# Kernel optimization log

Hardware: AMD Instinct MI355X
Metric: run time of the kernel (lower is better)

The kernel has to match this reference:

```python
import jax, jax.numpy as jnp
import numpy as np

FS = 5  # filter_size


def _extract_patches(x, fs):
    """x: (B, C, H, W) -> (B, C, fs*fs, H, W), 'same' padding, row-major
    shift order matching conv2d with an identity (one-hot) kernel."""
    B, C, H, W = x.shape
    pad = fs // 2
    xp = jnp.pad(x, ((0, 0), (0, 0), (pad, pad), (pad, pad)))
    shifts = [xp[:, :, i:i + H, j:j + W] for i in range(fs) for j in range(fs)]
    return jnp.stack(shifts, axis=2)


def setup_inputs() -> dict:
    key = jax.random.key(0)
    k1, k2 = jax.random.split(key)
    B, C, H, W = 8, 32, 128, 128
    x = jax.random.normal(k1, (B, C, H, W), dtype=jnp.float32)
    # PPDFGen modeled as a per-pixel linear map C -> fs^2 (1x1 conv) + bias
    w_gen = jax.random.normal(k2, (FS * FS, C), dtype=jnp.float32) * (1.0 / np.sqrt(C))
    b_gen = jnp.zeros((FS * FS,), dtype=jnp.float32)
    return {"x": x, "w_gen": w_gen, "b_gen": b_gen}


def reference(x, w_gen, b_gen):
    # Per-pixel dynamic filters: (B, fs^2, H, W)
    filters = jnp.einsum('bchw,fc->bfhw', x, w_gen) + b_gen[None, :, None, None]
    # Shifted patches (im2col via identity-kernel conv in the original):
    patches = _extract_patches(x, FS)            # (B, C, fs^2, H, W)
    # Elementwise multiply by filters (broadcast over channels) and reduce
    # over the fs^2 tap axis -- same math as the per-channel loop + concat.
    out = jnp.einsum('bcfhw,bfhw->bchw', patches, filters)
    return out
```

## Files before the change

### kernel.cpp

```cpp
#include <hip/hip_runtime.h>

#define FS   5
#define NTAP 25
#define Bc   8
#define Cc   32
#define Hc   128
#define Wc   128
#define HW   (Hc * Wc)

#define TH      8
#define TW      64
#define HALO_H  (TH + 4)
#define HALO_W  (TW + 4)
#define PLANE   (HALO_H * HALO_W)
#define NPAIR   (PLANE / 2)
#define LDS_BYTES (Cc * PLANE * 4)

__global__ __launch_bounds__(256, 1) void ppdfn_fused_kernel(
    const float* __restrict__ x, const float* __restrict__ wg,
    const float* __restrict__ bg, float* __restrict__ out)
{
    extern __shared__ float xs[];

    const int tid = threadIdx.x;
    const int ht  = blockIdx.x;
    const int wt  = blockIdx.y;
    const int b   = blockIdx.z;
    const int h0  = ht * TH;
    const int w0  = wt * TW;

    int  goff[2];
    bool val[2];
    bool st1;
#pragma unroll
    for (int k = 0; k < 2; ++k) {
        const int ip = tid + k * 256;
        const int i  = ip * 2;
        const int r  = i / HALO_W;
        const int cw = i - r * HALO_W;
        const int gh = h0 - 2 + r;
        const int gw = w0 - 2 + cw;
        val[k]  = (ip < NPAIR) && ((unsigned)gh < (unsigned)Hc) &&
                  ((unsigned)gw < (unsigned)Wc);
        goff[k] = gh * Wc + gw;
    }
    st1 = (tid < NPAIR - 256);

    const float* xb = x + (size_t)b * Cc * HW;

    for (int c = 0; c < Cc; ++c) {
        const float* xc = xb + (size_t)c * HW;
        float2 v0 = make_float2(0.f, 0.f), v1 = make_float2(0.f, 0.f);
        if (val[0]) v0 = *reinterpret_cast<const float2*>(xc + goff[0]);
        if (val[1]) v1 = *reinterpret_cast<const float2*>(xc + goff[1]);
        float* p = xs + c * PLANE;
        *reinterpret_cast<float2*>(p + 2 * tid) = v0;
        if (st1) *reinterpret_cast<float2*>(p + 2 * (tid + 256)) = v1;
    }
    __syncthreads();

    const int ty = tid >> 5;
    const int tx = tid & 31;
    const int w2 = tx * 2;

    float2 f[NTAP];
#pragma unroll
    for (int t = 0; t < NTAP; ++t) {
        const float bv = bg[t];
        f[t].x = bv; f[t].y = bv;
    }
#pragma unroll 2
    for (int c = 0; c < Cc; ++c) {
        const float2 xv = *reinterpret_cast<const float2*>(
            xs + c * PLANE + (ty + 2) * HALO_W + (w2 + 2));
#pragma unroll
        for (int t = 0; t < NTAP; ++t) {
            const float wv = wg[t * Cc + c];
            f[t].x = fmaf(wv, xv.x, f[t].x);
            f[t].y = fmaf(wv, xv.y, f[t].y);
        }
    }

    float* ob = out + (size_t)b * Cc * HW + (h0 + ty) * Wc + (w0 + w2);
#pragma unroll 2
    for (int c = 0; c < Cc; ++c) {
        const float* p = xs + c * PLANE + ty * HALO_W + w2;
        float accx = 0.f, accy = 0.f;
#pragma unroll
        for (int di = 0; di < FS; ++di) {
            const float* row = p + di * HALO_W;
            const float2 s01 = *reinterpret_cast<const float2*>(row);
            const float2 s23 = *reinterpret_cast<const float2*>(row + 2);
            const float2 s45 = *reinterpret_cast<const float2*>(row + 4);
            const float s0 = s01.x, s1 = s01.y, s2 = s23.x,
                        s3 = s23.y, s4 = s45.x, s5 = s45.y;
            const float2 f0 = f[di * FS + 0];
            const float2 f1 = f[di * FS + 1];
            const float2 f2 = f[di * FS + 2];
            const float2 f3 = f[di * FS + 3];
            const float2 f4 = f[di * FS + 4];
            accx = fmaf(f0.x, s0, accx);  accy = fmaf(f0.y, s1, accy);
            accx = fmaf(f1.x, s1, accx);  accy = fmaf(f1.y, s2, accy);
            accx = fmaf(f2.x, s2, accx);  accy = fmaf(f2.y, s3, accy);
            accx = fmaf(f3.x, s3, accx);  accy = fmaf(f3.y, s4, accy);
            accx = fmaf(f4.x, s4, accx);  accy = fmaf(f4.y, s5, accy);
        }
        *reinterpret_cast<float2*>(ob + (size_t)c * HW) = make_float2(accx, accy);
    }
}

extern "C" void kernel_launch(void* const* d_in, const int* in_sizes, int n_in,
                              void* d_out, int out_size, void* d_ws, size_t ws_size,
                              hipStream_t stream) {
    const float* x  = (const float*)d_in[0];
    const float* wg = (const float*)d_in[1];
    const float* bg = (const float*)d_in[2];
    float* out = (float*)d_out;

    ppdfn_fused_kernel<<<dim3(Hc / TH, Wc / TW, Bc), 256, LDS_BYTES, stream>>>(
        x, wg, bg, out);
}
```

Before: 28.05 us.

## Halve tile width to one pixel per thread and batch halo loads

Narrows the tile width from 64 to 32 so each thread computes one output pixel instead of two. This halves the LDS footprint and the filter registers per thread, and the launch bound now allows two blocks per CU, doubling the grid. The halo fill is restructured to issue eight channel loads before storing them to LDS, increasing memory-level parallelism. In exchange, the halo overhead per output rises, the global accesses are narrower, and the LDS reads become scalar rather than float2.

```diff
diff --git a/kernel.cpp b/kernel.cpp
--- a/kernel.cpp
+++ b/kernel.cpp
@@ -9,14 +9,14 @@
 #define HW   (Hc * Wc)
 
 #define TH      8
-#define TW      64
+#define TW      32
 #define HALO_H  (TH + 4)
 #define HALO_W  (TW + 4)
 #define PLANE   (HALO_H * HALO_W)
 #define NPAIR   (PLANE / 2)
 #define LDS_BYTES (Cc * PLANE * 4)
 
-__global__ __launch_bounds__(256, 1) void ppdfn_fused_kernel(
+__global__ __launch_bounds__(256, 2) void ppdfn_fused_kernel(
     const float* __restrict__ x, const float* __restrict__ wg,
     const float* __restrict__ bg, float* __restrict__ out)
 {
@@ -29,83 +29,72 @@
     const int h0  = ht * TH;
     const int w0  = wt * TW;
 
-    int  goff[2];
-    bool val[2];
-    bool st1;
-#pragma unroll
-    for (int k = 0; k < 2; ++k) {
-        const int ip = tid + k * 256;
-        const int i  = ip * 2;
-        const int r  = i / HALO_W;
-        const int cw = i - r * HALO_W;
-        const int gh = h0 - 2 + r;
-        const int gw = w0 - 2 + cw;
-        val[k]  = (ip < NPAIR) && ((unsigned)gh < (unsigned)Hc) &&
-                  ((unsigned)gw < (unsigned)Wc);
-        goff[k] = gh * Wc + gw;
-    }
-    st1 = (tid < NPAIR - 256);
+    const int i  = tid * 2;
+    const int r  = tid / 18;
+    const int cw = i - r * HALO_W;
+    const int gh = h0 - 2 + r;
+    const int gw = w0 - 2 + cw;
+    const bool val = (tid < NPAIR) && ((unsigned)gh < (unsigned)Hc) &&
+                     ((unsigned)gw < (unsigned)Wc);
+    const bool stv = (tid < NPAIR);
+    const int  go  = gh * Wc + gw;
 
     const float* xb = x + (size_t)b * Cc * HW;
 
-    for (int c = 0; c < Cc; ++c) {
-        const float* xc = xb + (size_t)c * HW;
-        float2 v0 = make_float2(0.f, 0.f), v1 = make_float2(0.f, 0.f);
-        if (val[0]) v0 = *reinterpret_cast<const float2*>(xc + goff[0]);
-        if (val[1]) v1 = *reinterpret_cast<const float2*>(xc + goff[1]);
-        float* p = xs + c * PLANE;
-        *reinterpret_cast<float2*>(p + 2 * tid) = v0;
-        if (st1) *reinterpret_cast<float2*>(p + 2 * (tid + 256)) = v1;
+#pragma unroll
+    for (int cg = 0; cg < Cc / 8; ++cg) {
+        float2 rv[8];
+#pragma unroll
+        for (int u = 0; u < 8; ++u) {
+            float2 v = make_float2(0.f, 0.f);
+            if (val)
+                v = *reinterpret_cast<const float2*>(
+                        xb + (size_t)(cg * 8 + u) * HW + go);
+            rv[u] = v;
+        }
+#pragma unroll
+        for (int u = 0; u < 8; ++u) {
+            if (stv)
+                *reinterpret_cast<float2*>(xs + (cg * 8 + u) * PLANE + i) = rv[u];
+        }
     }
     __syncthreads();
 
     const int ty = tid >> 5;
     const int tx = tid & 31;
-    const int w2 = tx * 2;
 
-    float2 f[NTAP];
+    float f[NTAP];
 #pragma unroll
-    for (int t = 0; t < NTAP; ++t) {
-        const float bv = bg[t];
-        f[t].x = bv; f[t].y = bv;
+    for (int t = 0; t < NTAP; ++t) f[t] = bg[t];
+
+#pragma unroll 4
+    for (int c = 0; c < Cc; ++c) {
+        const float xv = xs[c * PLANE + (ty + 2) * HALO_W + (tx + 2)];
+#pragma unroll
+        for (int t = 0; t < NTAP; ++t)
+            f[t] = fmaf(wg[t * Cc + c], xv, f[t]);
     }
+
+    float* ob = out + (size_t)b * Cc * HW + (h0 + ty) * Wc + (w0 + tx);
 #pragma unroll 2
     for (int c = 0; c < Cc; ++c) {
-        const float2 xv = *reinterpret_cast<const float2*>(
-            xs + c * PLANE + (ty + 2) * HALO_W + (w2 + 2));
-#pragma unroll
-        for (int t = 0; t < NTAP; ++t) {
-            const float wv = wg[t * Cc + c];
-            f[t].x = fmaf(wv, xv.x, f[t].x);
-            f[t].y = fmaf(wv, xv.y, f[t].y);
-        }
-    }
-
-    float* ob = out + (size_t)b * Cc * HW + (h0 + ty) * Wc + (w0 + w2);
-#pragma unroll 2
-    for (int c = 0; c < Cc; ++c) {
-        const float* p = xs + c * PLANE + ty * HALO_W + w2;
-        float accx = 0.f, accy = 0.f;
+        const float* p = xs + c * PLANE + ty * HALO_W + tx;
+        float acc = 0.f;
 #pragma unroll
         for (int di = 0; di < FS; ++di) {
             const float* row = p + di * HALO_W;
-            const float2 s01 = *reinterpret_cast<const float2*>(row);
-            const float2 s23 = *reinterpret_cast<const float2*>(row + 2);
-            const float2 s45 = *reinterpret_cast<const float2*>(row + 4);
-            const float s0 = s01.x, s1 = s01.y, s2 = s23.x,
-                        s3 = s23.y, s4 = s45.x, s5 = s45.y;
-            const float2 f0 = f[di * FS + 0];
-            const float2 f1 = f[di * FS + 1];
-            const float2 f2 = f[di * FS + 2];
-            const float2 f3 = f[di * FS + 3];
-            const float2 f4 = f[di * FS + 4];
-            accx = fmaf(f0.x, s0, accx);  accy = fmaf(f0.y, s1, accy);
-            accx = fmaf(f1.x, s1, accx);  accy = fmaf(f1.y, s2, accy);
-            accx = fmaf(f2.x, s2, accx);  accy = fmaf(f2.y, s3, accy);
-            accx = fmaf(f3.x, s3, accx);  accy = fmaf(f3.y, s4, accy);
-            accx = fmaf(f4.x, s4, accx);  accy = fmaf(f4.y, s5, accy);
+            const float s0 = row[0];
+            const float s1 = row[1];
+            const float s2 = row[2];
+            const float s3 = row[3];
+            const float s4 = row[4];
+            acc = fmaf(f[di * FS + 0], s0, acc);
+            acc = fmaf(f[di * FS + 1], s1, acc);
+            acc = fmaf(f[di * FS + 2], s2, acc);
+            acc = fmaf(f[di * FS + 3], s3, acc);
+            acc = fmaf(f[di * FS + 4], s4, acc);
         }
-        *reinterpret_cast<float2*>(ob + (size_t)c * HW) = make_float2(accx, accy);
+        ob[(size_t)c * HW] = acc;
     }
 }
 
```

New measurement: 24.07 us. -14.2%, faster.

## Split channels across two blocks per tile and batch halo loads in registers

Applied to the files above, without the earlier changes.

Each tile is now handled by two blocks, each staging only half the channels in LDS. That halves LDS use, allows two blocks per CU and doubles the grid to 512 blocks. The filter generation still needs all channels, so each block also reads the centre pixels of the other channel half straight from global memory. That duplicates some filter-generation FMAs and global reads. Halo loads are issued all at once into registers with masking rather than branches, and block IDs are remapped so neighbouring tiles share L2 locality.

```diff
diff --git a/kernel.cpp b/kernel.cpp
--- a/kernel.cpp
+++ b/kernel.cpp
@@ -1,61 +1,75 @@
 #include <hip/hip_runtime.h>
 
-#define FS   5
-#define NTAP 25
-#define Bc   8
-#define Cc   32
-#define Hc   128
-#define Wc   128
-#define HW   (Hc * Wc)
+#define FS    5
+#define NTAP  25
+#define Bc    8
+#define Cc    32
+#define CH    16
+#define Hc    128
+#define Wc    128
+#define HW    (Hc * Wc)
 
-#define TH      8
-#define TW      64
-#define HALO_H  (TH + 4)
-#define HALO_W  (TW + 4)
-#define PLANE   (HALO_H * HALO_W)
-#define NPAIR   (PLANE / 2)
-#define LDS_BYTES (Cc * PLANE * 4)
+#define TH    8
+#define TW    64
+#define HALO_H (TH + 4)
+#define HALO_W (TW + 4)
+#define PLANE  (HALO_H * HALO_W)
+#define NPAIR  (PLANE / 2)
+#define LDS_BYTES (CH * PLANE * 4)
 
-__global__ __launch_bounds__(256, 1) void ppdfn_fused_kernel(
+__global__ __launch_bounds__(256, 2) void ppdfn_fused(
     const float* __restrict__ x, const float* __restrict__ wg,
     const float* __restrict__ bg, float* __restrict__ out)
 {
     extern __shared__ float xs[];
+    const int tid = threadIdx.x;
+    const int bid = blockIdx.x;
 
-    const int tid = threadIdx.x;
-    const int ht  = blockIdx.x;
-    const int wt  = blockIdx.y;
-    const int b   = blockIdx.z;
-    const int h0  = ht * TH;
-    const int w0  = wt * TW;
+    const int g  = bid & 7;
+    const int m  = bid >> 3;
+    const int ht = (g << 1) + (m & 1);
+    const int wt = (m >> 1) & 1;
+    const int c0 = ((m >> 2) & 1) * CH;
+    const int b  = m >> 3;
 
-    int  goff[2];
-    bool val[2];
-    bool st1;
-#pragma unroll
-    for (int k = 0; k < 2; ++k) {
-        const int ip = tid + k * 256;
-        const int i  = ip * 2;
-        const int r  = i / HALO_W;
-        const int cw = i - r * HALO_W;
-        const int gh = h0 - 2 + r;
-        const int gw = w0 - 2 + cw;
-        val[k]  = (ip < NPAIR) && ((unsigned)gh < (unsigned)Hc) &&
-                  ((unsigned)gw < (unsigned)Wc);
-        goff[k] = gh * Wc + gw;
+    const int h0 = ht * TH, w0 = wt * TW;
+
+    const int ip0 = tid;
+    const int ip1 = tid + 256;
+    const bool s1ok = (ip1 < NPAIR);
+    int go0, go1; float m0, m1;
+    {
+        const int r  = ip0 / 34, pc = ip0 - r * 34;
+        const int gh = h0 - 2 + r, gw = w0 - 2 + 2 * pc;
+        const bool v = ((unsigned)gh < (unsigned)Hc) && ((unsigned)gw < (unsigned)Wc);
+        m0  = v ? 1.0f : 0.0f;
+        go0 = v ? gh * Wc + gw : 0;
     }
-    st1 = (tid < NPAIR - 256);
+    {
+        const int r  = ip1 / 34, pc = ip1 - r * 34;
+        const int gh = h0 - 2 + r, gw = w0 - 2 + 2 * pc;
+        const bool v = s1ok && ((unsigned)gh < (unsigned)Hc) && ((unsigned)gw < (unsigned)Wc);
+        m1  = v ? 1.0f : 0.0f;
+        go1 = v ? gh * Wc + gw : 0;
+    }
 
     const float* xb = x + (size_t)b * Cc * HW;
+    const float* xo = xb + (size_t)c0 * HW;
 
-    for (int c = 0; c < Cc; ++c) {
-        const float* xc = xb + (size_t)c * HW;
-        float2 v0 = make_float2(0.f, 0.f), v1 = make_float2(0.f, 0.f);
-        if (val[0]) v0 = *reinterpret_cast<const float2*>(xc + goff[0]);
-        if (val[1]) v1 = *reinterpret_cast<const float2*>(xc + goff[1]);
-        float* p = xs + c * PLANE;
-        *reinterpret_cast<float2*>(p + 2 * tid) = v0;
-        if (st1) *reinterpret_cast<float2*>(p + 2 * (tid + 256)) = v1;
+    float2 ra[CH], rb[CH];
+#pragma unroll
+    for (int c = 0; c < CH; ++c) {
+        ra[c] = *reinterpret_cast<const float2*>(xo + (size_t)c * HW + go0);
+        rb[c] = *reinterpret_cast<const float2*>(xo + (size_t)c * HW + go1);
+    }
+#pragma unroll
+    for (int c = 0; c < CH; ++c) {
+        float2 va = make_float2(ra[c].x * m0, ra[c].y * m0);
+        *reinterpret_cast<float2*>(xs + c * PLANE + 2 * ip0) = va;
+        if (s1ok) {
+            float2 vb = make_float2(rb[c].x * m1, rb[c].y * m1);
+            *reinterpret_cast<float2*>(xs + c * PLANE + 2 * ip1) = vb;
+        }
     }
     __syncthreads();
 
@@ -63,29 +77,46 @@
     const int tx = tid & 31;
     const int w2 = tx * 2;
 
-    float2 f[NTAP];
+    const int oc = c0 ^ CH;
+    const float* xc_other = xb + (size_t)oc * HW + (h0 + ty) * Wc + (w0 + w2);
+    float2 xv_o[CH];
 #pragma unroll
-    for (int t = 0; t < NTAP; ++t) {
-        const float bv = bg[t];
-        f[t].x = bv; f[t].y = bv;
-    }
-#pragma unroll 2
-    for (int c = 0; c < Cc; ++c) {
+    for (int c = 0; c < CH; ++c)
+        xv_o[c] = *reinterpret_cast<const float2*>(xc_other + (size_t)c * HW);
+
+    float fx[NTAP], fy[NTAP];
+#pragma unroll
+    for (int t = 0; t < NTAP; ++t) { const float bv = bg[t]; fx[t] = bv; fy[t] = bv; }
+
+#pragma unroll 4
+    for (int c = 0; c < CH; ++c) {
         const float2 xv = *reinterpret_cast<const float2*>(
             xs + c * PLANE + (ty + 2) * HALO_W + (w2 + 2));
+        const float* wrow = wg + (c0 + c);
 #pragma unroll
         for (int t = 0; t < NTAP; ++t) {
-            const float wv = wg[t * Cc + c];
-            f[t].x = fmaf(wv, xv.x, f[t].x);
-            f[t].y = fmaf(wv, xv.y, f[t].y);
+            const float wv = wrow[t * Cc];
+            fx[t] = fmaf(wv, xv.x, fx[t]);
+            fy[t] = fmaf(wv, xv.y, fy[t]);
+        }
+    }
+#pragma unroll 4
+    for (int c = 0; c < CH; ++c) {
+        const float2 xv = xv_o[c];
+        const float* wrow = wg + (oc + c);
+#pragma unroll
+        for (int t = 0; t < NTAP; ++t) {
+            const float wv = wrow[t * Cc];
+            fx[t] = fmaf(wv, xv.x, fx[t]);
+            fy[t] = fmaf(wv, xv.y, fy[t]);
         }
     }
 
-    float* ob = out + (size_t)b * Cc * HW + (h0 + ty) * Wc + (w0 + w2);
+    float* ob = out + ((size_t)b * Cc + c0) * HW + (h0 + ty) * Wc + (w0 + w2);
 #pragma unroll 2
-    for (int c = 0; c < Cc; ++c) {
+    for (int c = 0; c < CH; ++c) {
         const float* p = xs + c * PLANE + ty * HALO_W + w2;
-        float accx = 0.f, accy = 0.f;
+        float ax = 0.f, ay = 0.f;
 #pragma unroll
         for (int di = 0; di < FS; ++di) {
             const float* row = p + di * HALO_W;
@@ -94,18 +125,13 @@
             const float2 s45 = *reinterpret_cast<const float2*>(row + 4);
             const float s0 = s01.x, s1 = s01.y, s2 = s23.x,
                         s3 = s23.y, s4 = s45.x, s5 = s45.y;
-            const float2 f0 = f[di * FS + 0];
-            const float2 f1 = f[di * FS + 1];
-            const float2 f2 = f[di * FS + 2];
-            const float2 f3 = f[di * FS + 3];
-            const float2 f4 = f[di * FS + 4];
-            accx = fmaf(f0.x, s0, accx);  accy = fmaf(f0.y, s1, accy);
-            accx = fmaf(f1.x, s1, accx);  accy = fmaf(f1.y, s2, accy);
-            accx = fmaf(f2.x, s2, accx);  accy = fmaf(f2.y, s3, accy);
-            accx = fmaf(f3.x, s3, accx);  accy = fmaf(f3.y, s4, accy);
-            accx = fmaf(f4.x, s4, accx);  accy = fmaf(f4.y, s5, accy);
+            ax = fmaf(fx[di * FS + 0], s0, ax);  ay = fmaf(fy[di * FS + 0], s1, ay);
+            ax = fmaf(fx[di * FS + 1], s1, ax);  ay = fmaf(fy[di * FS + 1], s2, ay);
+            ax = fmaf(fx[di * FS + 2], s2, ax);  ay = fmaf(fy[di * FS + 2], s3, ay);
+            ax = fmaf(fx[di * FS + 3], s3, ax);  ay = fmaf(fy[di * FS + 3], s4, ay);
+            ax = fmaf(fx[di * FS + 4], s4, ax);  ay = fmaf(fy[di * FS + 4], s5, ay);
         }
-        *reinterpret_cast<float2*>(ob + (size_t)c * HW) = make_float2(accx, accy);
+        *reinterpret_cast<float2*>(ob + (size_t)c * HW) = make_float2(ax, ay);
     }
 }
 
@@ -117,6 +143,5 @@
     const float* bg = (const float*)d_in[2];
     float* out = (float*)d_out;
 
-    ppdfn_fused_kernel<<<dim3(Hc / TH, Wc / TW, Bc), 256, LDS_BYTES, stream>>>(
-        x, wg, bg, out);
+    ppdfn_fused<<<dim3(512), 256, LDS_BYTES, stream>>>(x, wg, bg, out);
 }
```

After: 26.84 us. 4.3% less time.

## Load halo tile via direct global-to-LDS 16-byte loads with widened row

Applied to the files above, without the earlier changes.

The halo staging now uses buffer/global_load_lds intrinsics that write 16-byte chunks from global memory straight into LDS, skipping the register round trip. To make 16-byte alignment work, each halo row is widened to 72 floats (4-column left pad), and out-of-bounds chunks read from a zero device buffer. Index offsets in the filter and aggregation loops are shifted to match, and the filter accumulators are split into separate x/y arrays. The wider plane raises LDS use and the zero buffer is assumed to be zero-initialized.

```diff
diff --git a/kernel.cpp b/kernel.cpp
--- a/kernel.cpp
+++ b/kernel.cpp
@@ -1,91 +1,94 @@
 #include <hip/hip_runtime.h>
 
-#define FS   5
-#define NTAP 25
-#define Bc   8
-#define Cc   32
-#define Hc   128
-#define Wc   128
-#define HW   (Hc * Wc)
+#define FS    5
+#define NTAP  25
+#define Bc    8
+#define Cc    32
+#define Hc    128
+#define Wc    128
+#define HW    (Hc * Wc)
 
 #define TH      8
 #define TW      64
-#define HALO_H  (TH + 4)
-#define HALO_W  (TW + 4)
+#define HALO_H  12
+#define HALO_W  72
 #define PLANE   (HALO_H * HALO_W)
-#define NPAIR   (PLANE / 2)
-#define LDS_BYTES (Cc * PLANE * 4)
+#define LDS_FLOATS (Cc * PLANE)
+#define LDS_BYTES  (LDS_FLOATS * 4)
+#define F4_PER_PLANE (PLANE / 4)
+#define F4_TOTAL     (Cc * F4_PER_PLANE)
+#define INSTR_TOTAL  (F4_TOTAL / 64)
+#define NWAVE        4
+#define INSTR_PER_WAVE (INSTR_TOTAL / NWAVE)
 
-__global__ __launch_bounds__(256, 1) void ppdfn_fused_kernel(
+__device__ __attribute__((aligned(16))) float ZERO4[4];
+
+__device__ __forceinline__ void gload_lds16(const float* g, float* lds) {
+    __builtin_amdgcn_global_load_lds(
+        (const __attribute__((address_space(1))) void*)g,
+        (__attribute__((address_space(3))) void*)lds, 16, 0, 0);
+}
+
+__global__ __launch_bounds__(256, 1) void ppdfn_fused(
     const float* __restrict__ x, const float* __restrict__ wg,
     const float* __restrict__ bg, float* __restrict__ out)
 {
     extern __shared__ float xs[];
 
-    const int tid = threadIdx.x;
-    const int ht  = blockIdx.x;
-    const int wt  = blockIdx.y;
-    const int b   = blockIdx.z;
-    const int h0  = ht * TH;
-    const int w0  = wt * TW;
-
-    int  goff[2];
-    bool val[2];
-    bool st1;
-#pragma unroll
-    for (int k = 0; k < 2; ++k) {
-        const int ip = tid + k * 256;
-        const int i  = ip * 2;
-        const int r  = i / HALO_W;
-        const int cw = i - r * HALO_W;
-        const int gh = h0 - 2 + r;
-        const int gw = w0 - 2 + cw;
-        val[k]  = (ip < NPAIR) && ((unsigned)gh < (unsigned)Hc) &&
-                  ((unsigned)gw < (unsigned)Wc);
-        goff[k] = gh * Wc + gw;
-    }
-    st1 = (tid < NPAIR - 256);
+    const int tid  = threadIdx.x;
+    const int lane = tid & 63;
+    const int wv   = tid >> 6;
+    const int ht   = blockIdx.x;
+    const int wt   = blockIdx.y;
+    const int b    = blockIdx.z;
+    const int h0   = ht * TH;
+    const int w0   = wt * TW;
 
     const float* xb = x + (size_t)b * Cc * HW;
 
-    for (int c = 0; c < Cc; ++c) {
-        const float* xc = xb + (size_t)c * HW;
-        float2 v0 = make_float2(0.f, 0.f), v1 = make_float2(0.f, 0.f);
-        if (val[0]) v0 = *reinterpret_cast<const float2*>(xc + goff[0]);
-        if (val[1]) v1 = *reinterpret_cast<const float2*>(xc + goff[1]);
-        float* p = xs + c * PLANE;
-        *reinterpret_cast<float2*>(p + 2 * tid) = v0;
-        if (st1) *reinterpret_cast<float2*>(p + 2 * (tid + 256)) = v1;
+    const int f_base = wv * (INSTR_PER_WAVE * 64) + lane;
+#pragma unroll
+    for (int k = 0; k < INSTR_PER_WAVE; ++k) {
+        const int f  = f_base + k * 64;
+        const int c  = f / F4_PER_PLANE;
+        const int rm = f - c * F4_PER_PLANE;
+        const int r  = rm / 18;
+        const int c4 = rm - r * 18;
+        const int gh = h0 - 2 + r;
+        const int gw = w0 - 4 + 4 * c4;
+        const bool v = ((unsigned)gh < (unsigned)Hc) &&
+                       ((unsigned)gw <= (unsigned)(Wc - 4));
+        const float* src = v ? (xb + (size_t)c * HW + gh * Wc + gw) : ZERO4;
+        gload_lds16(src, xs + (size_t)(wv * INSTR_PER_WAVE + k) * 256);
     }
+    asm volatile("s_waitcnt vmcnt(0)" ::: "memory");
     __syncthreads();
 
     const int ty = tid >> 5;
     const int tx = tid & 31;
     const int w2 = tx * 2;
 
-    float2 f[NTAP];
+    float fx[NTAP], fy[NTAP];
 #pragma unroll
-    for (int t = 0; t < NTAP; ++t) {
-        const float bv = bg[t];
-        f[t].x = bv; f[t].y = bv;
-    }
-#pragma unroll 2
+    for (int t = 0; t < NTAP; ++t) { const float bv = bg[t]; fx[t] = bv; fy[t] = bv; }
+
+#pragma unroll 4
     for (int c = 0; c < Cc; ++c) {
         const float2 xv = *reinterpret_cast<const float2*>(
-            xs + c * PLANE + (ty + 2) * HALO_W + (w2 + 2));
+            xs + c * PLANE + (ty + 2) * HALO_W + (w2 + 4));
 #pragma unroll
         for (int t = 0; t < NTAP; ++t) {
-            const float wv = wg[t * Cc + c];
-            f[t].x = fmaf(wv, xv.x, f[t].x);
-            f[t].y = fmaf(wv, xv.y, f[t].y);
+            const float wv_ = wg[t * Cc + c];
+            fx[t] = fmaf(wv_, xv.x, fx[t]);
+            fy[t] = fmaf(wv_, xv.y, fy[t]);
         }
     }
 
     float* ob = out + (size_t)b * Cc * HW + (h0 + ty) * Wc + (w0 + w2);
 #pragma unroll 2
     for (int c = 0; c < Cc; ++c) {
-        const float* p = xs + c * PLANE + ty * HALO_W + w2;
-        float accx = 0.f, accy = 0.f;
+        const float* p = xs + c * PLANE + ty * HALO_W + (w2 + 2);
+        float ax = 0.f, ay = 0.f;
 #pragma unroll
         for (int di = 0; di < FS; ++di) {
             const float* row = p + di * HALO_W;
@@ -94,18 +97,13 @@
             const float2 s45 = *reinterpret_cast<const float2*>(row + 4);
             const float s0 = s01.x, s1 = s01.y, s2 = s23.x,
                         s3 = s23.y, s4 = s45.x, s5 = s45.y;
-            const float2 f0 = f[di * FS + 0];
-            const float2 f1 = f[di * FS + 1];
-            const float2 f2 = f[di * FS + 2];
-            const float2 f3 = f[di * FS + 3];
-            const float2 f4 = f[di * FS + 4];
-            accx = fmaf(f0.x, s0, accx);  accy = fmaf(f0.y, s1, accy);
-            accx = fmaf(f1.x, s1, accx);  accy = fmaf(f1.y, s2, accy);
-            accx = fmaf(f2.x, s2, accx);  accy = fmaf(f2.y, s3, accy);
-            accx = fmaf(f3.x, s3, accx);  accy = fmaf(f3.y, s4, accy);
-            accx = fmaf(f4.x, s4, accx);  accy = fmaf(f4.y, s5, accy);
+            ax = fmaf(fx[di * FS + 0], s0, ax);  ay = fmaf(fy[di * FS + 0], s1, ay);
+            ax = fmaf(fx[di * FS + 1], s1, ax);  ay = fmaf(fy[di * FS + 1], s2, ay);
+            ax = fmaf(fx[di * FS + 2], s2, ax);  ay = fmaf(fy[di * FS + 2], s3, ay);
+            ax = fmaf(fx[di * FS + 3], s3, ax);  ay = fmaf(fy[di * FS + 3], s4, ay);
+            ax = fmaf(fx[di * FS + 4], s4, ax);  ay = fmaf(fy[di * FS + 4], s5, ay);
         }
-        *reinterpret_cast<float2*>(ob + (size_t)c * HW) = make_float2(accx, accy);
+        *reinterpret_cast<float2*>(ob + (size_t)c * HW) = make_float2(ax, ay);
     }
 }
 
@@ -117,6 +115,6 @@
     const float* bg = (const float*)d_in[2];
     float* out = (float*)d_out;
 
-    ppdfn_fused_kernel<<<dim3(Hc / TH, Wc / TW, Bc), 256, LDS_BYTES, stream>>>(
+    ppdfn_fused<<<dim3(Hc / TH, Wc / TW, Bc), 256, LDS_BYTES, stream>>>(
         x, wg, bg, out);
 }
```

Result: faster. 23.24 us (-17.2%).
